# Kernel tuning notes

Measured on AMD Instinct MI355X. Metric: run time of the kernel, lower is better.

The kernel has to match this reference:

```python
import jax, jax.numpy as jnp
import numpy as np
from jax import lax

P = 16      # n_features
H = 24      # hidden size (hard-coded in module)
B = 8192
T = 168


def setup_inputs() -> dict:
    key = jax.random.key(0)
    ks = jax.random.split(key, 8)
    s_ih = 1.0 / np.sqrt(H)
    return {
        "x": jax.random.normal(ks[0], (B, T, P), dtype=jnp.float32),
        # PyTorch LSTM params: gate order [i, f, g, o], uniform(-1/sqrt(H), 1/sqrt(H))
        "W_ih": jax.random.uniform(ks[1], (4 * H, P), jnp.float32, -s_ih, s_ih),
        "W_hh": jax.random.uniform(ks[2], (4 * H, H), jnp.float32, -s_ih, s_ih),
        "b_ih": jax.random.uniform(ks[3], (4 * H,), jnp.float32, -s_ih, s_ih),
        "b_hh": jax.random.uniform(ks[4], (4 * H,), jnp.float32, -s_ih, s_ih),
        "W_lin": jax.random.uniform(ks[5], (H, H), jnp.float32, -s_ih, s_ih),
        "b_lin": jax.random.uniform(ks[6], (H,), jnp.float32, -s_ih, s_ih),
    }


def _lstm_last_h(x, W_ih, W_hh, b_ih, b_hh):
    # Precompute input-side gate pre-activations for all timesteps: [B, T, 4H]
    xg = jnp.einsum("btp,gp->btg", x, W_ih) + (b_ih + b_hh)
    W_hh_T = W_hh.T  # [H, 4H]
    Bsz = x.shape[0]
    h0 = jnp.zeros((Bsz, H), dtype=x.dtype)
    c0 = jnp.zeros((Bsz, H), dtype=x.dtype)

    def step(carry, xt):
        h, c = carry
        g = xt + h @ W_hh_T  # [B, 4H]
        i = jax.nn.sigmoid(g[:, 0 * H:1 * H])
        f = jax.nn.sigmoid(g[:, 1 * H:2 * H])
        gg = jnp.tanh(g[:, 2 * H:3 * H])
        o = jax.nn.sigmoid(g[:, 3 * H:4 * H])
        c = f * c + i * gg
        h = o * jnp.tanh(c)
        return (h, c), None

    (h_last, _), _ = lax.scan(step, (h0, c0), jnp.swapaxes(xg, 0, 1))
    return h_last  # [B, H]


def reference(x, W_ih, W_hh, b_ih, b_hh, W_lin, b_lin):
    h_last = _lstm_last_h(x, W_ih, W_hh, b_ih, b_hh)
    # tanh over LSTM outputs, then linear head on the last timestep
    out = jnp.tanh(h_last) @ W_lin.T + b_lin  # [B, H]
    return out.reshape(out.shape[0], -1, 1)   # [B, 24, 1]
```

## Files before the change

### kernel.cpp

```cpp
#include <hip/hip_runtime.h>


#define T_STEPS 168
#define P_FEAT  16
#define H_SZ    24
#define TCH     84
#define NB      16

typedef _Float16 half8 __attribute__((ext_vector_type(8)));
typedef _Float16 h2    __attribute__((ext_vector_type(2)));
typedef float    f32x4 __attribute__((ext_vector_type(4)));

__device__ __forceinline__ float rcp_fast(float x) {
#if __has_builtin(__builtin_amdgcn_rcpf)
    return __builtin_amdgcn_rcpf(x);
#else
    return 1.0f / x;
#endif
}
__device__ __forceinline__ float exp2_fast(float x) {
#if __has_builtin(__builtin_amdgcn_exp2f)
    return __builtin_amdgcn_exp2f(x);
#else
    return exp2f(x);
#endif
}
__device__ __forceinline__ float sigmoid_f(float x) {
    return rcp_fast(1.0f + exp2_fast(x * -1.44269504f));
}
__device__ __forceinline__ float tanh_f(float x) {
    return 1.0f - 2.0f * rcp_fast(1.0f + exp2_fast(x * 2.88539008f));
}
__device__ __forceinline__ h2 pack2(float a, float b) {
    h2 r; r.x = (_Float16)a; r.y = (_Float16)b; return r;
}

__global__ __launch_bounds__(128, 1) void lstm_sp(
    const float* __restrict__ x,
    const float* __restrict__ W_ih,
    const float* __restrict__ W_hh,
    const float* __restrict__ b_ih,
    const float* __restrict__ b_hh,
    const float* __restrict__ W_lin,
    const float* __restrict__ b_lin,
    float* __restrict__ out)
{
    __shared__ __align__(16) _Float16 xs16[NB][TCH][16];
    __shared__ __align__(16) _Float16 hpad[2][NB][40];
    __shared__ __align__(16) _Float16 zblk[16];
    __shared__ __align__(16) float    thbuf[NB][24];

    const int tid  = threadIdx.x;
    const int w    = tid >> 6;
    const int lane = tid & 63;
    const int n    = lane & 15;
    const int quad = lane >> 4;

    float* wstage = reinterpret_cast<float*>(&xs16[0][0][0]);
    for (int idx = tid; idx < 96 * 40; idx += 128) {
        const int j = idx / 40;
        const int k = idx - j * 40;
        wstage[idx] = (k < 24) ? W_hh[j * 24 + k] : W_ih[j * 16 + (k - 24)];
    }
    __syncthreads();

    half8 A1[3], A2[3];
    f32x4 biasf[3];
    #pragma unroll
    for (int s = 0; s < 3; s++) {
        const int mt   = w * 3 + s;
        const int grow = (n & 3) * 24 + (n >> 2) * 6 + mt;
        #pragma unroll
        for (int j = 0; j < 8; j++) {
            const int k = quad * 8 + j;
            A1[s][j] = (k < 24) ? (_Float16)wstage[grow * 40 + k] : (_Float16)0.0f;
            A2[s][j] = (k < 16) ? (_Float16)wstage[grow * 40 + 24 + k] : (_Float16)0.0f;
        }
        #pragma unroll
        for (int r = 0; r < 4; r++) {
            const int row = r * 24 + quad * 6 + mt;
            biasf[s][r] = b_ih[row] + b_hh[row];
        }
    }
    __syncthreads();

    {
        unsigned* hz = reinterpret_cast<unsigned*>(&hpad[0][0][0]);
        for (int i = tid; i < 640; i += 128) hz[i] = 0u;
        if (tid < 8) reinterpret_cast<unsigned*>(zblk)[tid] = 0u;
    }
    __syncthreads();

    float c[3] = {0, 0, 0};
    float hv[3] = {0, 0, 0};

    const float4* xsrc = reinterpret_cast<const float4*>(x)
                       + (size_t)(blockIdx.x * NB) * (T_STEPS * P_FEAT / 4);

    const _Float16* xrowbase = (quad < 2) ? &xs16[n][0][quad * 8] : zblk;
    const int xstep = (quad < 2) ? 16 : 0;

    int bufp = 0;
    for (int ch = 0; ch < 2; ch++) {
        for (int i = 0; i < 42; i++) {
            const int m   = tid + 128 * i;
            const int b   = m / 336;
            const int rem = m - b * 336;
            const float4 v = xsrc[(size_t)b * (T_STEPS * P_FEAT / 4) + ch * 336 + rem];
            h2* dst = reinterpret_cast<h2*>(&xs16[0][0][0]) + b * 672 + rem * 2;
            dst[0] = pack2(v.x, v.y);
            dst[1] = pack2(v.z, v.w);
        }
        __syncthreads();

        f32x4 gx[3];
        {
            const half8 B2 = *reinterpret_cast<const half8*>(xrowbase);
            #pragma unroll
            for (int s = 0; s < 3; s++)
                gx[s] = __builtin_amdgcn_mfma_f32_16x16x32_f16(A2[s], B2, biasf[s], 0, 0, 0);
        }

        for (int t = 0; t < TCH; t++) {
            const half8 B1 = *reinterpret_cast<const half8*>(&hpad[bufp][n][quad * 8]);
            const int  tn  = (t + 1 < TCH) ? t + 1 : 0;
            const half8 B2n = *reinterpret_cast<const half8*>(xrowbase + tn * xstep);

            f32x4 g[3];
            #pragma unroll
            for (int s = 0; s < 3; s++)
                g[s] = __builtin_amdgcn_mfma_f32_16x16x32_f16(A1[s], B1, gx[s], 0, 0, 0);

            #pragma unroll
            for (int s = 0; s < 3; s++)
                gx[s] = __builtin_amdgcn_mfma_f32_16x16x32_f16(A2[s], B2n, biasf[s], 0, 0, 0);

            #pragma unroll
            for (int s = 0; s < 3; s++) {
                const float ig = sigmoid_f(g[s][0]);
                const float fg = sigmoid_f(g[s][1]);
                const float gg = tanh_f   (g[s][2]);
                const float og = sigmoid_f(g[s][3]);
                c[s]  = fg * c[s] + ig * gg;
                hv[s] = og * tanh_f(c[s]);
            }

            const int u0 = quad * 6 + w * 3;
            hpad[1 - bufp][n][u0 + 0] = (_Float16)hv[0];
            hpad[1 - bufp][n][u0 + 1] = (_Float16)hv[1];
            hpad[1 - bufp][n][u0 + 2] = (_Float16)hv[2];

            bufp ^= 1;
            __syncthreads();
        }
    }

    {
        const int u0 = quad * 6 + w * 3;
        #pragma unroll
        for (int s = 0; s < 3; s++) thbuf[n][u0 + s] = tanh_f(hv[s]);
    }
    __syncthreads();

    float th[24];
    #pragma unroll
    for (int kk = 0; kk < 6; kk++) {
        const f32x4 t4 = *reinterpret_cast<const f32x4*>(&thbuf[n][4 * kk]);
        th[4 * kk + 0] = t4[0]; th[4 * kk + 1] = t4[1];
        th[4 * kk + 2] = t4[2]; th[4 * kk + 3] = t4[3];
    }
    const int batch = blockIdx.x * NB + n;
    #pragma unroll
    for (int s = 0; s < 3; s++) {
        const int j = quad * 6 + w * 3 + s;
        const float* wl = &W_lin[j * 24];
        float acc = b_lin[j];
        #pragma unroll
        for (int k = 0; k < 24; k++) acc = fmaf(th[k], wl[k], acc);
        out[(size_t)batch * 24 + j] = acc;
    }
}

extern "C" void kernel_launch(void* const* d_in, const int* in_sizes, int n_in,
                              void* d_out, int out_size, void* d_ws, size_t ws_size,
                              hipStream_t stream) {
    const float* x     = (const float*)d_in[0];
    const float* W_ih  = (const float*)d_in[1];
    const float* W_hh  = (const float*)d_in[2];
    const float* b_ih  = (const float*)d_in[3];
    const float* b_hh  = (const float*)d_in[4];
    const float* W_lin = (const float*)d_in[5];
    const float* b_lin = (const float*)d_in[6];
    float* out = (float*)d_out;

    const int B = in_sizes[0] / (T_STEPS * P_FEAT);
    dim3 grid(B / NB), block(128);
    lstm_sp<<<grid, block, 0, stream>>>(x, W_ih, W_hh, b_ih, b_hh, W_lin, b_lin, out);
}
```

Before: 234.2 us.

## Split per-block LSTM recurrence across four waves instead of two

Each 16-sequence block now uses four wavefronts instead of two, so each wave handles two hidden units (two MFMA tiles) per step instead of three. This shortens each wave's per-step MFMA and activation chain on the serial recurrence. The gate-row mapping is rearranged with padded rows (12 of 16 used) and h is exchanged through a packed half2 LDS buffer. In exchange, some MFMA lanes do wasted work, more waves join the per-step barrier, and block occupancy and LDS pressure change.

```diff
diff --git a/kernel.cpp b/kernel.cpp
--- a/kernel.cpp
+++ b/kernel.cpp
@@ -35,7 +35,7 @@
     h2 r; r.x = (_Float16)a; r.y = (_Float16)b; return r;
 }
 
-__global__ __launch_bounds__(128, 1) void lstm_sp(
+__global__ __launch_bounds__(256, 2) void lstm_4w(
     const float* __restrict__ x,
     const float* __restrict__ W_ih,
     const float* __restrict__ W_hh,
@@ -46,97 +46,99 @@
     float* __restrict__ out)
 {
     __shared__ __align__(16) _Float16 xs16[NB][TCH][16];
-    __shared__ __align__(16) _Float16 hpad[2][NB][40];
-    __shared__ __align__(16) _Float16 zblk[16];
+    __shared__ __align__(16) h2       hx[2][4][NB][4];
+    __shared__ __align__(16) h2       zblk[8];
     __shared__ __align__(16) float    thbuf[NB][24];
 
     const int tid  = threadIdx.x;
     const int w    = tid >> 6;
     const int lane = tid & 63;
     const int n    = lane & 15;
-    const int quad = lane >> 4;
+    const int q    = lane >> 4;
 
     float* wstage = reinterpret_cast<float*>(&xs16[0][0][0]);
-    for (int idx = tid; idx < 96 * 40; idx += 128) {
+    for (int idx = tid; idx < 96 * 40; idx += 256) {
         const int j = idx / 40;
         const int k = idx - j * 40;
         wstage[idx] = (k < 24) ? W_hh[j * 24 + k] : W_ih[j * 16 + (k - 24)];
     }
     __syncthreads();
 
-    half8 A1[3], A2[3];
-    f32x4 biasf[3];
+    half8 A1[2], A2[2];
+    f32x4 biasf[2];
     #pragma unroll
-    for (int s = 0; s < 3; s++) {
-        const int mt   = w * 3 + s;
-        const int grow = (n & 3) * 24 + (n >> 2) * 6 + mt;
+    for (int s = 0; s < 2; s++) {
+        const int mt = 2 * w + s;
+        const int p  = n;
+        const bool vrow = (p < 12);
+        const int grow = vrow ? ((p & 3) * 24 + 8 * (p >> 2) + mt) : 0;
         #pragma unroll
         for (int j = 0; j < 8; j++) {
-            const int k = quad * 8 + j;
-            A1[s][j] = (k < 24) ? (_Float16)wstage[grow * 40 + k] : (_Float16)0.0f;
-            A2[s][j] = (k < 16) ? (_Float16)wstage[grow * 40 + 24 + k] : (_Float16)0.0f;
+            const int k = q * 8 + j;
+            A1[s][j] = (vrow && k < 24) ? (_Float16)wstage[grow * 40 + k]      : (_Float16)0.0f;
+            A2[s][j] = (vrow && k < 16) ? (_Float16)wstage[grow * 40 + 24 + k] : (_Float16)0.0f;
         }
         #pragma unroll
         for (int r = 0; r < 4; r++) {
-            const int row = r * 24 + quad * 6 + mt;
-            biasf[s][r] = b_ih[row] + b_hh[row];
+            const int u = 8 * q + mt;
+            biasf[s][r] = (q < 3) ? (b_ih[r * 24 + u] + b_hh[r * 24 + u]) : 0.0f;
         }
     }
     __syncthreads();
 
     {
-        unsigned* hz = reinterpret_cast<unsigned*>(&hpad[0][0][0]);
-        for (int i = tid; i < 640; i += 128) hz[i] = 0u;
+        unsigned* hz = reinterpret_cast<unsigned*>(&hx[0][0][0][0]);
+        for (int i = tid; i < 512; i += 256) hz[i] = 0u;
         if (tid < 8) reinterpret_cast<unsigned*>(zblk)[tid] = 0u;
     }
     __syncthreads();
 
-    float c[3] = {0, 0, 0};
-    float hv[3] = {0, 0, 0};
+    float c[2] = {0.0f, 0.0f};
+    float hv[2] = {0.0f, 0.0f};
 
     const float4* xsrc = reinterpret_cast<const float4*>(x)
                        + (size_t)(blockIdx.x * NB) * (T_STEPS * P_FEAT / 4);
 
-    const _Float16* xrowbase = (quad < 2) ? &xs16[n][0][quad * 8] : zblk;
-    const int xstep = (quad < 2) ? 16 : 0;
+    const _Float16* xrowbase = (q < 2) ? &xs16[n][0][q * 8]
+                                       : reinterpret_cast<const _Float16*>(zblk);
+    const int xstep = (q < 2) ? 16 : 0;
 
     int bufp = 0;
     for (int ch = 0; ch < 2; ch++) {
-        for (int i = 0; i < 42; i++) {
-            const int m   = tid + 128 * i;
+        for (int i = 0; i < 21; i++) {
+            const int m   = tid + 256 * i;
             const int b   = m / 336;
             const int rem = m - b * 336;
-            const float4 v = xsrc[(size_t)b * (T_STEPS * P_FEAT / 4) + ch * 336 + rem];
+            const float4 v = xsrc[(size_t)b * 672 + ch * 336 + rem];
             h2* dst = reinterpret_cast<h2*>(&xs16[0][0][0]) + b * 672 + rem * 2;
             dst[0] = pack2(v.x, v.y);
             dst[1] = pack2(v.z, v.w);
         }
         __syncthreads();
 
-        f32x4 gx[3];
+        f32x4 gx[2];
         {
             const half8 B2 = *reinterpret_cast<const half8*>(xrowbase);
             #pragma unroll
-            for (int s = 0; s < 3; s++)
+            for (int s = 0; s < 2; s++)
                 gx[s] = __builtin_amdgcn_mfma_f32_16x16x32_f16(A2[s], B2, biasf[s], 0, 0, 0);
         }
 
         for (int t = 0; t < TCH; t++) {
-            const half8 B1 = *reinterpret_cast<const half8*>(&hpad[bufp][n][quad * 8]);
-            const int  tn  = (t + 1 < TCH) ? t + 1 : 0;
+            const half8 B1 = *reinterpret_cast<const half8*>(&hx[bufp][q][n][0]);
+            const int tn = (t + 1 < TCH) ? t + 1 : 0;
             const half8 B2n = *reinterpret_cast<const half8*>(xrowbase + tn * xstep);
 
-            f32x4 g[3];
+            f32x4 g[2];
             #pragma unroll
-            for (int s = 0; s < 3; s++)
+            for (int s = 0; s < 2; s++)
                 g[s] = __builtin_amdgcn_mfma_f32_16x16x32_f16(A1[s], B1, gx[s], 0, 0, 0);
-
             #pragma unroll
-            for (int s = 0; s < 3; s++)
+            for (int s = 0; s < 2; s++)
                 gx[s] = __builtin_amdgcn_mfma_f32_16x16x32_f16(A2[s], B2n, biasf[s], 0, 0, 0);
 
             #pragma unroll
-            for (int s = 0; s < 3; s++) {
+            for (int s = 0; s < 2; s++) {
                 const float ig = sigmoid_f(g[s][0]);
                 const float fg = sigmoid_f(g[s][1]);
                 const float gg = tanh_f   (g[s][2]);
@@ -145,39 +147,29 @@
                 hv[s] = og * tanh_f(c[s]);
             }
 
-            const int u0 = quad * 6 + w * 3;
-            hpad[1 - bufp][n][u0 + 0] = (_Float16)hv[0];
-            hpad[1 - bufp][n][u0 + 1] = (_Float16)hv[1];
-            hpad[1 - bufp][n][u0 + 2] = (_Float16)hv[2];
-
+            if (q < 3) hx[1 - bufp][q][n][w] = pack2(hv[0], hv[1]);
             bufp ^= 1;
             __syncthreads();
         }
     }
 
-    {
-        const int u0 = quad * 6 + w * 3;
-        #pragma unroll
-        for (int s = 0; s < 3; s++) thbuf[n][u0 + s] = tanh_f(hv[s]);
+    if (q < 3) {
+        thbuf[n][8 * q + 2 * w + 0] = tanh_f(hv[0]);
+        thbuf[n][8 * q + 2 * w + 1] = tanh_f(hv[1]);
     }
     __syncthreads();
 
-    float th[24];
-    #pragma unroll
-    for (int kk = 0; kk < 6; kk++) {
-        const f32x4 t4 = *reinterpret_cast<const f32x4*>(&thbuf[n][4 * kk]);
-        th[4 * kk + 0] = t4[0]; th[4 * kk + 1] = t4[1];
-        th[4 * kk + 2] = t4[2]; th[4 * kk + 3] = t4[3];
-    }
-    const int batch = blockIdx.x * NB + n;
-    #pragma unroll
-    for (int s = 0; s < 3; s++) {
-        const int j = quad * 6 + w * 3 + s;
-        const float* wl = &W_lin[j * 24];
-        float acc = b_lin[j];
+    if (q < 3) {
+        const int batch = blockIdx.x * NB + n;
         #pragma unroll
-        for (int k = 0; k < 24; k++) acc = fmaf(th[k], wl[k], acc);
-        out[(size_t)batch * 24 + j] = acc;
+        for (int s = 0; s < 2; s++) {
+            const int u = 8 * q + 2 * w + s;
+            const float* wl = &W_lin[u * 24];
+            float acc = b_lin[u];
+            #pragma unroll
+            for (int k = 0; k < 24; k++) acc = fmaf(thbuf[n][k], wl[k], acc);
+            out[(size_t)batch * 24 + u] = acc;
+        }
     }
 }
 
@@ -194,6 +186,6 @@
     float* out = (float*)d_out;
 
     const int B = in_sizes[0] / (T_STEPS * P_FEAT);
-    dim3 grid(B / NB), block(128);
-    lstm_sp<<<grid, block, 0, stream>>>(x, W_ih, W_hh, b_ih, b_hh, W_lin, b_lin, out);
+    dim3 grid(B / NB), block(256);
+    lstm_4w<<<grid, block, 0, stream>>>(x, W_ih, W_hh, b_ih, b_hh, W_lin, b_lin, out);
 }
```

Result: faster. 203.2 us (-13.2%).
